# Kernel optimization log

Measured on AMD Instinct MI355X. Metric: run time of the kernel, lower is better.

The kernel has to match this reference:

```python
import jax, jax.numpy as jnp
import numpy as np
from jax import lax

B, T = 4, 2048
IN_CH, SKIP_CH, OUT_CH, K = 256, 128, 128, 5
N_MAMBA, D_STATE, D_CONV, EXPAND = 2, 16, 4, 2
D_INNER = EXPAND * OUT_CH
DT_RANK = (OUT_CH + 15) // 16  # ceil(d_model/16) = 8
L = 2 * T
EPS = 1e-5


def setup_inputs() -> dict:
    key = jax.random.key(0)
    ks = jax.random.split(key, 16)
    def rn(k, shape, s=0.02):
        return jax.random.normal(k, shape, jnp.float32) * s
    A_init = jnp.broadcast_to(jnp.arange(1, D_STATE + 1, dtype=jnp.float32),
                              (N_MAMBA, 2, D_INNER, D_STATE))
    return {
        'x': rn(ks[0], (B, IN_CH, T), 1.0),
        'skip': rn(ks[1], (B, SKIP_CH, L), 1.0),
        'up_w': rn(ks[2], (IN_CH, IN_CH, K)),       # torch ConvTranspose1d weight (in,out,k)
        'up_b': jnp.zeros((IN_CH,), jnp.float32),
        'fus_w': rn(ks[3], (OUT_CH, IN_CH + SKIP_CH)),  # 1x1 conv
        'fus_b': jnp.zeros((OUT_CH,), jnp.float32),
        'gn_w': jnp.ones((OUT_CH,), jnp.float32),
        'gn_b': jnp.zeros((OUT_CH,), jnp.float32),
        'prelu_a': jnp.array(0.25, jnp.float32),
        'ln_w': jnp.ones((N_MAMBA, OUT_CH), jnp.float32),
        'ln_b': jnp.zeros((N_MAMBA, OUT_CH), jnp.float32),
        'in_w': rn(ks[4], (N_MAMBA, 2, 2 * D_INNER, OUT_CH)),
        'conv_w': rn(ks[5], (N_MAMBA, 2, D_INNER, D_CONV), 0.1),
        'conv_b': jnp.zeros((N_MAMBA, 2, D_INNER), jnp.float32),
        'xproj_w': rn(ks[6], (N_MAMBA, 2, DT_RANK + 2 * D_STATE, D_INNER)),
        'dtproj_w': rn(ks[7], (N_MAMBA, 2, D_INNER, DT_RANK), 0.1),
        'dtproj_b': rn(ks[8], (N_MAMBA, 2, D_INNER), 0.1),
        'A_log': jnp.log(A_init),
        'Dp': jnp.ones((N_MAMBA, 2, D_INNER), jnp.float32),
        'out_w': rn(ks[9], (N_MAMBA, 2, OUT_CH, D_INNER)),
    }


def _mamba_branch(xn, cw, cb, iw, xw, dw, db, Alog, Dp, ow):
    # xn: [B, L, d_model] -> [B, L, d_model]; standard Mamba selective scan.
    xz = jnp.einsum('bld,ed->ble', xn, iw)            # [B,L,2*D_INNER]
    xi, z = jnp.split(xz, 2, axis=-1)
    # causal depthwise conv over time
    xc = lax.conv_general_dilated(xi.transpose(0, 2, 1), cw[:, None, :], (1,),
                                  [(D_CONV - 1, 0)], feature_group_count=D_INNER,
                                  dimension_numbers=('NCH', 'OIH', 'NCH'))
    xi = jax.nn.silu(xc + cb[None, :, None]).transpose(0, 2, 1)  # [B,L,D_INNER]
    dbl = jnp.einsum('bld,ed->ble', xi, xw)           # [B,L,DT_RANK+2N]
    dt = jax.nn.softplus(jnp.einsum('blr,dr->bld', dbl[..., :DT_RANK], dw) + db)
    Bc = dbl[..., DT_RANK:DT_RANK + D_STATE]          # [B,L,N]
    Cc = dbl[..., DT_RANK + D_STATE:]                 # [B,L,N]
    A = -jnp.exp(Alog)                                # [D_INNER,N]
    dA = jnp.exp(dt[..., None] * A)                   # [B,L,D_INNER,N]
    dBx = dt[..., None] * Bc[:, :, None, :] * xi[..., None]
    def comb(c1, c2):
        a1, b1 = c1
        a2, b2 = c2
        return a1 * a2, a2 * b1 + b2
    _, h = lax.associative_scan(comb, (dA, dBx), axis=1)  # h_t = dA_t h_{t-1} + dBx_t
    y = jnp.einsum('bldn,bln->bld', h, Cc) + Dp * xi
    return jnp.einsum('ble,de->bld', y * jax.nn.silu(z), ow)


def _forward(x, skip, up_w, up_b, fus_w, fus_b, gn_w, gn_b, prelu_a, ln_w, ln_b,
             in_w, conv_w, conv_b, xproj_w, dtproj_w, dtproj_b, A_log, Dp, out_w):
    p = K // 2
    # ConvTranspose1d(stride=2, padding=p, output_padding=1) == lhs-dilated conv with flipped kernel
    wt = jnp.flip(up_w, -1).transpose(1, 0, 2)        # (out,in,k)
    u = lax.conv_general_dilated(x, wt, (1,), [(K - 1 - p, K - 1 - p + 1)],
                                 lhs_dilation=(2,),
                                 dimension_numbers=('NCH', 'OIH', 'NCH'))
    u = u + up_b[None, :, None]
    u = u[..., :skip.shape[-1]]
    h = jnp.concatenate([u, skip], axis=1)            # [B, in+skip, L]
    h = jnp.einsum('bct,oc->bot', h, fus_w) + fus_b[None, :, None]
    # GroupNorm(1, C): normalize over (C,T) per sample
    mu = h.mean(axis=(1, 2), keepdims=True)
    var = h.var(axis=(1, 2), keepdims=True)
    h = (h - mu) / jnp.sqrt(var + EPS) * gn_w[None, :, None] + gn_b[None, :, None]
    h = jnp.where(h >= 0, h, prelu_a * h)             # PReLU (single param)
    h = h.transpose(0, 2, 1)                          # [B, L, C]
    for i in range(N_MAMBA):
        # BiMambaBlock: pre-LN, forward + time-reversed Mamba, residual sum
        mu2 = h.mean(-1, keepdims=True)
        v2 = h.var(-1, keepdims=True)
        xn = (h - mu2) / jnp.sqrt(v2 + EPS) * ln_w[i] + ln_b[i]
        f = _mamba_branch(xn, conv_w[i, 0], conv_b[i, 0], in_w[i, 0], xproj_w[i, 0],
                          dtproj_w[i, 0], dtproj_b[i, 0], A_log[i, 0], Dp[i, 0], out_w[i, 0])
        b = _mamba_branch(jnp.flip(xn, 1), conv_w[i, 1], conv_b[i, 1], in_w[i, 1], xproj_w[i, 1],
                          dtproj_w[i, 1], dtproj_b[i, 1], A_log[i, 1], Dp[i, 1], out_w[i, 1])
        h = h + f + jnp.flip(b, 1)
    return h.transpose(0, 2, 1)                       # [B, C_out, L]


def reference(x, skip, up_w, up_b, fus_w, fus_b, gn_w, gn_b, prelu_a, ln_w, ln_b,
              in_w, conv_w, conv_b, xproj_w, dtproj_w, dtproj_b, A_log, Dp, out_w):
    return _forward(x, skip, up_w, up_b, fus_w, fus_b, gn_w, gn_b, prelu_a, ln_w, ln_b,
                    in_w, conv_w, conv_b, xproj_w, dtproj_w, dtproj_b, A_log, Dp, out_w)
```

## Files before the change

kernel.cpp:

```cpp
#include <hip/hip_runtime.h>
#include <hip/hip_bf16.h>

#define Bsz 4
#define Tt 2048
#define Ll 4096
#define NC 256
#define CH 16
#define NG 16

typedef short bf16x8 __attribute__((ext_vector_type(8)));
typedef float f32x4 __attribute__((ext_vector_type(4)));
typedef float f32x2 __attribute__((ext_vector_type(2)));

static __device__ __forceinline__ f32x2 pk_fma(f32x2 a, f32x2 b, f32x2 c){
  f32x2 d;
  asm("v_pk_fma_f32 %0, %1, %2, %3" : "=v"(d) : "v"(a), "v"(b), "v"(c));
  return d;
}
static __device__ __forceinline__ f32x2 pk_mul(f32x2 a, f32x2 b){
  f32x2 d;
  asm("v_pk_mul_f32 %0, %1, %2" : "=v"(d) : "v"(a), "v"(b));
  return d;
}
static __device__ __forceinline__ f32x2 lo2(f32x4 v){ return (f32x2){v.x, v.y}; }
static __device__ __forceinline__ f32x2 hi2(f32x4 v){ return (f32x2){v.z, v.w}; }

static __device__ __forceinline__ float bs2f(unsigned short u){
  union{float f; unsigned int i;} v; v.i = ((unsigned int)u)<<16; return v.f;
}
static __device__ __forceinline__ unsigned short f2bs(float f){
  union{float f; unsigned int i;} v; v.f = f;
  unsigned int r = (v.i + 0x7fffu + ((v.i>>16)&1u)) >> 16;
  return (unsigned short)r;
}

__global__ void k_cvt(const float* __restrict__ src, unsigned short* __restrict__ dst, int n){
  int i = blockIdx.x*256 + threadIdx.x;
  if (i < n) dst[i] = f2bs(src[i]);
}

__global__ void k_prepx(const float* __restrict__ xw, unsigned short* __restrict__ wxb){
  int row = blockIdx.x, br = blockIdx.y, col = threadIdx.x;
  float v = (row < 40) ? xw[((size_t)br*40 + row)*256 + col] : 0.f;
  wxb[((size_t)br*64 + row)*256 + col] = f2bs(v);
}

__global__ void k_prepA(const float* __restrict__ Alog, float* __restrict__ AEX,
                        float* __restrict__ A0C, float* __restrict__ CHN){
  int br = blockIdx.x, d = threadIdx.x;
  float A[16];
  #pragma unroll
  for (int j=0;j<4;j++){
    float4 a4 = *(const float4*)&Alog[(size_t)br*4096 + d*16 + j*4];
    A[4*j]  = -__expf(a4.x); A[4*j+1] = -__expf(a4.y);
    A[4*j+2]= -__expf(a4.z); A[4*j+3] = -__expf(a4.w);
    *(float4*)&AEX[(size_t)br*4096 + d*16 + j*4] = (float4){A[4*j],A[4*j+1],A[4*j+2],A[4*j+3]};
  }
  bool chain = true;
  #pragma unroll
  for (int n=1;n<16;n++){
    float expect = A[0]*(float)(n+1);
    if (fabsf(A[n]-expect) > 1e-3f*fabsf(expect)) chain = false;
  }
  A0C[br*256 + d] = A[0];
  CHN[br*256 + d] = chain ? 1.f : 0.f;
}

__global__ void k_compose(const float* __restrict__ up_w, const float* __restrict__ fus_w,
                          const float* __restrict__ fus_b, const float* __restrict__ up_b,
                          unsigned short* __restrict__ WEb, unsigned short* __restrict__ WOb,
                          unsigned short* __restrict__ FWSb, float* __restrict__ BIAS2){
  int i = blockIdx.x;
  int o = threadIdx.x;
  float a0=0.f,a1=0.f,a2=0.f,a3=0.f,a4=0.f;
  for (int c=0;c<256;c++){
    float f = fus_w[o*384+c];
    const float* w = up_w + ((size_t)i*256+c)*5;
    a0 += f*w[0]; a1 += f*w[1]; a2 += f*w[2];
    a3 += f*w[3]; a4 += f*w[4];
  }
  WEb[(size_t)o*768 +       i] = f2bs(a4);
  WEb[(size_t)o*768 + 256 + i] = f2bs(a2);
  WEb[(size_t)o*768 + 512 + i] = f2bs(a0);
  WOb[(size_t)o*512 +       i] = f2bs(a3);
  WOb[(size_t)o*512 + 256 + i] = f2bs(a1);
  if (i<128) FWSb[o*128 + i] = f2bs(fus_w[o*384+256+i]);
  if (i==0){
    float bb = fus_b[o];
    for (int c=0;c<256;c++) bb += fus_w[o*384+c]*up_b[c];
    BIAS2[o]=bb;
  }
}

__global__ __launch_bounds__(256) void k_tx(const float* __restrict__ x, unsigned short* __restrict__ XT){
  __shared__ float tile[64][65];
  int b=blockIdx.z, t0=blockIdx.x*64, i0=blockIdx.y*64;
  int tid=threadIdx.x;
  for (int it=0;it<16;it++){
    int idx=it*256+tid; int ii=idx>>6, tt=idx&63;
    tile[ii][tt] = x[((size_t)b*256+i0+ii)*Tt + t0+tt];
  }
  __syncthreads();
  for (int it=0;it<16;it++){
    int idx=it*256+tid; int tt=idx>>6, ii=idx&63;
    XT[((size_t)b*2050 + t0+tt+1)*256 + i0+ii] = f2bs(tile[ii][tt]);
  }
}

__global__ void k_zero(unsigned short* __restrict__ XT){
  int tid=threadIdx.x;
  for (int b=0;b<Bsz;b++){
    XT[((size_t)b*2050)*256 + tid] = 0;
    XT[((size_t)b*2050+2049)*256 + tid] = 0;
  }
}

__global__ __launch_bounds__(256) void k_ts(const float* __restrict__ skip, unsigned short* __restrict__ SKT){
  __shared__ float tile[64][65];
  int b=blockIdx.z, l0=blockIdx.x*64, s0=blockIdx.y*64;
  int tid=threadIdx.x;
  for (int it=0;it<16;it++){
    int idx=it*256+tid; int ss=idx>>6, ll=idx&63;
    tile[ss][ll] = skip[((size_t)b*128+s0+ss)*Ll + l0+ll];
  }
  __syncthreads();
  for (int it=0;it<16;it++){
    int idx=it*256+tid; int ll=idx>>6, ss=idx&63;
    SKT[((size_t)b*Ll + l0+ll)*128 + s0+ss] = f2bs(tile[ss][ll]);
  }
}

__global__ __launch_bounds__(256) void k_up(const unsigned short* __restrict__ XT,
                     const unsigned short* __restrict__ SKT,
                     const unsigned short* __restrict__ WEb, const unsigned short* __restrict__ WOb,
                     const unsigned short* __restrict__ FWSb, const float* __restrict__ B2,
                     float* __restrict__ h0, float* __restrict__ gst){
  __shared__ unsigned short XL[66*264];
  __shared__ unsigned short Wb[128*72];
  __shared__ float red0[256], red1[256];
  int bt = blockIdx.x, par = blockIdx.y, b = blockIdx.z;
  int t0 = bt*64;
  int tid = threadIdx.x;
  int wave = tid>>6, lane = tid&63;
  int wm = wave>>1, wn = wave&1;
  int quad = lane>>4, l16 = lane&15;

  for (int idx=tid; idx<66*32; idx+=256){
    int row = idx>>5, c8 = idx&31;
    *(uint4*)&XL[row*264 + c8*8] = *(const uint4*)&XT[((size_t)b*2050 + t0 + row)*256 + c8*8];
  }

  const unsigned short* Wsrc = par ? WOb : WEb;
  const int Kw = par ? 512 : 768;
  const int tapbase = par ? 1 : 0;
  f32x4 acc[2][4];
  #pragma unroll
  for (int i=0;i<2;i++)
    #pragma unroll
    for (int j=0;j<4;j++) acc[i][j] = (f32x4){0.f,0.f,0.f,0.f};

  int nch = Kw>>6;
  for (int kc=0; kc<nch; kc++){
    __syncthreads();
    #pragma unroll
    for (int it=0; it<4; it++){
      int idx = it*256+tid;
      int row = idx>>3, c8 = idx&7;
      *(uint4*)&Wb[row*72 + c8*8] = *(const uint4*)&Wsrc[(size_t)row*Kw + kc*64 + c8*8];
    }
    __syncthreads();
    #pragma unroll
    for (int ks=0; ks<64; ks+=32){
      int kg = kc*64 + ks;
      int tap = kg>>8, ib = kg&255;
      bf16x8 af[2], bf[4];
      #pragma unroll
      for (int mt=0;mt<2;mt++)
        af[mt] = *(bf16x8*)&XL[(wm*32+mt*16+l16 + tapbase + tap)*264 + ib + quad*8];
      #pragma unroll
      for (int nt=0;nt<4;nt++)
        bf[nt] = *(bf16x8*)&Wb[(wn*64+nt*16+l16)*72 + ks + quad*8];
      #pragma unroll
      for (int mt=0;mt<2;mt++)
        #pragma unroll
        for (int nt=0;nt<4;nt++)
          acc[mt][nt] = __builtin_amdgcn_mfma_f32_16x16x32_bf16(af[mt], bf[nt], acc[mt][nt], 0,0,0);
    }
  }

  __syncthreads();
  for (int idx=tid; idx<64*16; idx+=256){
    int row = idx>>4, c8 = idx&15;
    *(uint4*)&XL[row*136 + c8*8] = *(const uint4*)&SKT[((size_t)b*Ll + 2*(t0+row)+par)*128 + c8*8];
  }
  for (int kc=0; kc<2; kc++){
    __syncthreads();
    #pragma unroll
    for (int it=0; it<4; it++){
      int idx = it*256+tid;
      int row = idx>>3, c8 = idx&7;
      *(uint4*)&Wb[row*72 + c8*8] = *(const uint4*)&FWSb[(size_t)row*128 + kc*64 + c8*8];
    }
    __syncthreads();
    #pragma unroll
    for (int ks=0; ks<64; ks+=32){
      bf16x8 af[2], bf[4];
      #pragma unroll
      for (int mt=0;mt<2;mt++)
        af[mt] = *(bf16x8*)&XL[(wm*32+mt*16+l16)*136 + kc*64 + ks + quad*8];
      #pragma unroll
      for (int nt=0;nt<4;nt++)
        bf[nt] = *(bf16x8*)&Wb[(wn*64+nt*16+l16)*72 + ks + quad*8];
      #pragma unroll
      for (int mt=0;mt<2;mt++)
        #pragma unroll
        for (int nt=0;nt<4;nt++)
          acc[mt][nt] = __builtin_amdgcn_mfma_f32_16x16x32_bf16(af[mt], bf[nt], acc[mt][nt], 0,0,0);
    }
  }

  float s1=0.f, s2=0.f;
  #pragma unroll
  for (int mt=0;mt<2;mt++)
    #pragma unroll
    for (int nt=0;nt<4;nt++)
      #pragma unroll
      for (int r=0;r<4;r++){
        int m = wm*32 + mt*16 + quad*4 + r;
        int lrow = 2*(t0+m) + par;
        int col = wn*64 + nt*16 + l16;
        float v = acc[mt][nt][r] + B2[col];
        h0[((size_t)b*Ll + lrow)*128 + col] = v;
        s1 += v; s2 += v*v;
      }
  red0[tid]=s1; red1[tid]=s2;
  __syncthreads();
  for (int st=128; st>0; st>>=1){
    if (tid<st){ red0[tid]+=red0[tid+st]; red1[tid]+=red1[tid+st]; }
    __syncthreads();
  }
  if (tid==0){ atomicAdd(&gst[b*2], red0[0]); atomicAdd(&gst[b*2+1], red1[0]); }
}

__global__ void k_gnfin(float* gst){
  int b = threadIdx.x;
  if (b < Bsz){
    float n = (float)Ll*128.f;
    float mu = gst[b*2]/n;
    float var = gst[b*2+1]/n - mu*mu;
    gst[8+b]=mu; gst[12+b]=rsqrtf(var+1e-5f);
  }
}

__global__ __launch_bounds__(256) void k_gnln(const float* __restrict__ h0, const float* __restrict__ gn_w,
                      const float* __restrict__ gn_b, const float* __restrict__ pa,
                      const float* __restrict__ gst, const float* __restrict__ lnw,
                      const float* __restrict__ lnb, float* __restrict__ hres,
                      unsigned short* __restrict__ xn){
  int row = blockIdx.x*4 + (threadIdx.x>>6);
  int lane = threadIdx.x & 63;
  int b = row >> 12;
  float mu_g = gst[8+b], inv_g = gst[12+b];
  float a = pa[0];
  const float* hp = h0 + (size_t)row*128;
  float u0 = (hp[lane]   -mu_g)*inv_g*gn_w[lane]    + gn_b[lane];
  float u1 = (hp[lane+64]-mu_g)*inv_g*gn_w[lane+64] + gn_b[lane+64];
  float v0 = u0>=0.f ? u0 : a*u0;
  float v1 = u1>=0.f ? u1 : a*u1;
  float* rp = hres + (size_t)row*128;
  rp[lane] = v0; rp[lane+64] = v1;
  float s = v0+v1, q = v0*v0+v1*v1;
  #pragma unroll
  for (int off=32; off>0; off>>=1){
    s += __shfl_xor(s, off, 64);
    q += __shfl_xor(q, off, 64);
  }
  float mu = s*(1.f/128.f);
  float rs = rsqrtf(q*(1.f/128.f)-mu*mu + 1e-5f);
  unsigned short* xp = xn + (size_t)row*128;
  xp[lane]    = f2bs((v0-mu)*rs*lnw[lane]    + lnb[lane]);
  xp[lane+64] = f2bs((v1-mu)*rs*lnw[lane+64] + lnb[lane+64]);
}

__global__ __launch_bounds__(256) void k_gemm_in(const unsigned short* __restrict__ A,
                          const unsigned short* __restrict__ W,
                          unsigned short* __restrict__ C){
  __shared__ unsigned short As[128*72];
  __shared__ unsigned short Bs[128*72];
  int tid = threadIdx.x;
  int row0 = blockIdx.x*128;
  int n0   = blockIdx.y*128;
  int dir  = blockIdx.z;
  const unsigned short* Wp = W + (size_t)dir*512*128;
  unsigned short* Cp = C + (size_t)dir*Bsz*Ll*512;
  int wave = tid>>6, lane = tid&63;
  int wm = wave>>1, wn = wave&1;
  int quad = lane>>4, l16 = lane&15;
  f32x4 acc[4][4];
  #pragma unroll
  for (int i=0;i<4;i++)
    #pragma unroll
    for (int j=0;j<4;j++) acc[i][j] = (f32x4){0.f,0.f,0.f,0.f};

  for (int kb=0; kb<128; kb+=64){
    __syncthreads();
    #pragma unroll
    for (int it=0; it<4; it++){
      int idx = it*256 + tid;
      int row = idx>>3, c8 = idx&7;
      int r = row0 + row;
      int p = r & (Ll-1); int bb = r >> 12;
      int src = (bb<<12) + (dir ? (Ll-1-p) : p);
      *(uint4*)&As[row*72 + c8*8] = *(const uint4*)&A[(size_t)src*128 + kb + c8*8];
      *(uint4*)&Bs[row*72 + c8*8] = *(const uint4*)&Wp[(size_t)(n0+row)*128 + kb + c8*8];
    }
    __syncthreads();
    #pragma unroll
    for (int ks=0; ks<64; ks+=32){
      bf16x8 af[4], bf[4];
      #pragma unroll
      for (int mt=0;mt<4;mt++)
        af[mt] = *(bf16x8*)&As[(wm*64+mt*16+l16)*72 + ks + quad*8];
      #pragma unroll
      for (int nt=0;nt<4;nt++)
        bf[nt] = *(bf16x8*)&Bs[(wn*64+nt*16+l16)*72 + ks + quad*8];
      #pragma unroll
      for (int mt=0;mt<4;mt++)
        #pragma unroll
        for (int nt=0;nt<4;nt++)
          acc[mt][nt] = __builtin_amdgcn_mfma_f32_16x16x32_bf16(af[mt], bf[nt], acc[mt][nt], 0,0,0);
    }
  }
  #pragma unroll
  for (int mt=0;mt<4;mt++)
    #pragma unroll
    for (int nt=0;nt<4;nt++)
      #pragma unroll
      for (int r=0;r<4;r++){
        int row = row0 + wm*64 + mt*16 + quad*4 + r;
        int col = n0 + wn*64 + nt*16 + l16;
        Cp[(size_t)row*512 + col] = f2bs(acc[mt][nt][r]);
      }
}

template<int DO_LN>
__global__ __launch_bounds__(256) void k_gemm_out_t(const unsigned short* __restrict__ Y,
                           const unsigned short* __restrict__ W,
                           float* __restrict__ C, const float* __restrict__ lnw,
                           const float* __restrict__ lnb, unsigned short* __restrict__ xn){
  __shared__ unsigned short As[64*72];
  __shared__ unsigned short Bs[128*72];
  __shared__ float redS[2][4][2][4][2][2];
  int tid = threadIdx.x;
  int row0 = blockIdx.x*64;
  int wave = tid>>6, lane = tid&63;
  int wm = wave>>1, wn = wave&1;
  int quad = lane>>4, l16 = lane&15;
  const size_t planeY = (size_t)Bsz*Ll*256;
  f32x4 acc[2][4];
  #pragma unroll
  for (int i=0;i<2;i++)
    #pragma unroll
    for (int j=0;j<4;j++) acc[i][j] = (f32x4){0.f,0.f,0.f,0.f};

  for (int kc=0; kc<8; kc++){
    int dirp = kc>>2;
    int kb = (kc&3)*64;
    const unsigned short* Wp = W + (size_t)dirp*128*256;
    __syncthreads();
    #pragma unroll
    for (int it=0; it<2; it++){
      int idx = it*256 + tid;
      int row = idx>>3, c8 = idx&7;
      int r = row0 + row;
      int p = r & (Ll-1); int bb = r >> 12;
      int srow = dirp ? ((bb<<12) + (Ll-1-p)) : r;
      *(uint4*)&As[row*72 + c8*8] = *(const uint4*)&Y[dirp*planeY + (size_t)srow*256 + kb + c8*8];
    }
    #pragma unroll
    for (int it=0; it<4; it++){
      int idx = it*256 + tid;
      int row = idx>>3, c8 = idx&7;
      *(uint4*)&Bs[row*72 + c8*8] = *(const uint4*)&Wp[(size_t)row*256 + kb + c8*8];
    }
    __syncthreads();
    #pragma unroll
    for (int ks=0; ks<64; ks+=32){
      bf16x8 af[2], bf[4];
      #pragma unroll
      for (int mt=0;mt<2;mt++)
        af[mt] = *(bf16x8*)&As[(wm*32+mt*16+l16)*72 + ks + quad*8];
      #pragma unroll
      for (int nt=0;nt<4;nt++)
        bf[nt] = *(bf16x8*)&Bs[(wn*64+nt*16+l16)*72 + ks + quad*8];
      #pragma unroll
      for (int mt=0;mt<2;mt++)
        #pragma unroll
        for (int nt=0;nt<4;nt++)
          acc[mt][nt] = __builtin_amdgcn_mfma_f32_16x16x32_bf16(af[mt], bf[nt], acc[mt][nt], 0,0,0);
    }
  }

  float vals[2][4][4];
  #pragma unroll
  for (int mt=0;mt<2;mt++)
    #pragma unroll
    for (int nt=0;nt<4;nt++)
      #pragma unroll
      for (int r=0;r<4;r++){
        int row = row0 + wm*32 + mt*16 + quad*4 + r;
        int col = wn*64 + nt*16 + l16;
        float v = C[(size_t)row*128 + col] + acc[mt][nt][r];
        C[(size_t)row*128 + col] = v;
        vals[mt][nt][r] = v;
      }

  if (DO_LN){
    #pragma unroll
    for (int mt=0;mt<2;mt++)
      #pragma unroll
      for (int r=0;r<4;r++){
        float s = 0.f, q = 0.f;
        #pragma unroll
        for (int nt=0;nt<4;nt++){ float v = vals[mt][nt][r]; s += v; q += v*v; }
        #pragma unroll
        for (int off=1; off<16; off<<=1){
          s += __shfl_xor(s, off, 64);
          q += __shfl_xor(q, off, 64);
        }
        if (l16 == 0){
          redS[wm][quad][mt][r][wn][0] = s;
          redS[wm][quad][mt][r][wn][1] = q;
        }
      }
    __syncthreads();
    #pragma unroll
    for (int mt=0;mt<2;mt++)
      #pragma unroll
      for (int r=0;r<4;r++){
        float s = redS[wm][quad][mt][r][0][0] + redS[wm][quad][mt][r][1][0];
        float q = redS[wm][quad][mt][r][0][1] + redS[wm][quad][mt][r][1][1];
        float mu = s*(1.f/128.f);
        float rs = rsqrtf(q*(1.f/128.f) - mu*mu + 1e-5f);
        int row = row0 + wm*32 + mt*16 + quad*4 + r;
        #pragma unroll
        for (int nt=0;nt<4;nt++){
          int col = wn*64 + nt*16 + l16;
          xn[(size_t)row*128 + col] = f2bs((vals[mt][nt][r]-mu)*rs*lnw[col] + lnb[col]);
        }
      }
  }
}

__global__ __launch_bounds__(256) void k_xproj3(const unsigned short* __restrict__ xz,
                        const unsigned short* __restrict__ wxb,
                        const float* __restrict__ cw, const float* __restrict__ cb,
                        unsigned short* __restrict__ xib, float* __restrict__ dbl){
  __shared__ unsigned short xiS[64*264];
  __shared__ unsigned short Bs[64*72];
  int tid = threadIdx.x;
  int dir = blockIdx.y;
  xz  += (size_t)dir*Bsz*Ll*512;
  wxb += (size_t)dir*64*256;
  cw  += dir*1024;
  cb  += dir*256;
  xib += (size_t)dir*Bsz*Ll*256;
  dbl += (size_t)dir*Bsz*Ll*40;
  size_t row0 = (size_t)blockIdx.x*64;
  int p0 = (int)(row0 & (Ll-1));

  {
    int d = tid;
    float4 w4 = *(const float4*)&cw[d*4];
    float bias = cb[d];
    float w0, w1, w2;
    if (p0 == 0){ w0=0.f; w1=0.f; w2=0.f; }
    else {
      w0 = bs2f(xz[(row0-3)*512 + d]);
      w1 = bs2f(xz[(row0-2)*512 + d]);
      w2 = bs2f(xz[(row0-1)*512 + d]);
    }
    #pragma unroll 4
    for (int rr=0; rr<64; rr++){
      float xv = bs2f(xz[(row0+rr)*512 + d]);
      float acc = bias + w4.x*w0 + w4.y*w1 + w4.z*w2 + w4.w*xv;
      float v = acc*__builtin_amdgcn_rcpf(1.f+__expf(-acc));
      unsigned short us = f2bs(v);
      xiS[rr*264 + d] = us;
      xib[(row0+rr)*256 + d] = us;
      w0=w1; w1=w2; w2=xv;
    }
  }

  int wave = tid>>6, lane = tid&63;
  int quad = lane>>4, l16 = lane&15;
  f32x4 acc[4];
  #pragma unroll
  for (int j=0;j<4;j++) acc[j] = (f32x4){0.f,0.f,0.f,0.f};

  for (int kb=0; kb<256; kb+=64){
    __syncthreads();
    #pragma unroll
    for (int it=0; it<2; it++){
      int idx = it*256 + tid;
      int row = idx>>3, c8 = idx&7;
      *(uint4*)&Bs[row*72 + c8*8] = *(const uint4*)&wxb[(size_t)row*256 + kb + c8*8];
    }
    __syncthreads();
    #pragma unroll
    for (int ks=0; ks<64; ks+=32){
      bf16x8 af = *(bf16x8*)&xiS[(wave*16+l16)*264 + kb + ks + quad*8];
      #pragma unroll
      for (int nt=0;nt<4;nt++){
        bf16x8 bf = *(bf16x8*)&Bs[(nt*16+l16)*72 + ks + quad*8];
        acc[nt] = __builtin_amdgcn_mfma_f32_16x16x32_bf16(af, bf, acc[nt], 0,0,0);
      }
    }
  }
  #pragma unroll
  for (int nt=0;nt<4;nt++)
    #pragma unroll
    for (int r=0;r<4;r++){
      int m = wave*16 + quad*4 + r;
      int col = nt*16 + l16;
      if (col < 40) dbl[(row0+m)*40 + col] = acc[nt][r];
    }
}

#define POWTREE2(e1, pw2) { \
  float _e2 = (e1)*(e1); \
  f32x2 _e2v = (f32x2){_e2,_e2}; \
  pw2[0] = (f32x2){(e1),_e2}; \
  pw2[1] = pk_mul(pw2[0], _e2v); \
  pw2[2] = pk_mul(pw2[1], _e2v); \
  pw2[3] = pk_mul(pw2[2], _e2v); \
  f32x2 _e8v = (f32x2){pw2[3].y, pw2[3].y}; \
  pw2[4] = pk_mul(pw2[0], _e8v); \
  pw2[5] = pk_mul(pw2[1], _e8v); \
  pw2[6] = pk_mul(pw2[2], _e8v); \
  pw2[7] = pk_mul(pw2[3], _e8v); }

__global__ __launch_bounds__(256) void k_scan1(const float* __restrict__ dbl,
                       const unsigned short* __restrict__ xib, const float* __restrict__ AEX,
                       const float* __restrict__ A0C, const float* __restrict__ CHNf,
                       const float* __restrict__ dtw, const float* __restrict__ dtb,
                       float* __restrict__ SD, float* __restrict__ Q){
  __shared__ float dblS[CH*24];
  int b = blockIdx.y, c = blockIdx.x, dir = blockIdx.z;
  int d = threadIdx.x;
  const float* dblP = dbl + (size_t)dir*Bsz*Ll*40;
  const unsigned short* xiP = xib + (size_t)dir*Bsz*Ll*256;
  size_t base = (size_t)b*Ll + (size_t)c*CH;
  if (d < CH*6){
    int p = d/6, j = d - p*6;
    *(float4*)&dblS[p*24 + j*4] = *(const float4*)&dblP[(base+p)*40 + j*4];
  }
  float A0 = A0C[dir*256 + d];
  bool chain = CHNf[dir*256 + d] != 0.f;
  f32x2 wv2[4];
  {
    const float* dw = dtw + (size_t)dir*2048 + d*8;
    float4 w0 = *(const float4*)&dw[0];
    float4 w1 = *(const float4*)&dw[4];
    wv2[0]=(f32x2){w0.x,w0.y}; wv2[1]=(f32x2){w0.z,w0.w};
    wv2[2]=(f32x2){w1.x,w1.y}; wv2[3]=(f32x2){w1.z,w1.w};
  }
  float bbt = dtb[dir*256 + d];
  __syncthreads();
  float sdt = 0.f;
  const unsigned short* xip = xiP + base*256 + d;
  size_t sbase = (size_t)dir*Bsz*NC*4096 + ((size_t)(b*NC + c))*4096 + (size_t)d*16;
  if (chain){
    bool n1 = fabsf(A0 + 1.f) < 1e-6f;
    float xv[CH];
    #pragma unroll
    for (int p=0;p<CH;p++) xv[p] = bs2f(xip[(size_t)p*256]);
    f32x2 h2[8];
    #pragma unroll
    for (int i=0;i<8;i++) h2[i] = (f32x2){0.f,0.f};
    #pragma unroll
    for (int p=0;p<CH;p++){
      const float* rw = &dblS[p*24];
      f32x4 t0 = *(const f32x4*)&rw[0];
      f32x4 t1 = *(const f32x4*)&rw[4];
      f32x2 dp = pk_mul(lo2(t0), wv2[0]);
      dp = pk_fma(hi2(t0), wv2[1], dp);
      dp = pk_fma(lo2(t1), wv2[2], dp);
      dp = pk_fma(hi2(t1), wv2[3], dp);
      float a0 = bbt + dp.x + dp.y;
      float t = __expf(a0);
      float u = 1.f + t;
      float dtv = (a0>20.f)? a0 : __logf(u);
      float e1 = n1 ? __builtin_amdgcn_rcpf(u) : __expf(dtv*A0);
      float dx = dtv*xv[p];
      sdt += dtv;
      f32x2 pw2[8];
      POWTREE2(e1, pw2);
      f32x2 dxv = (f32x2){dx,dx};
      f32x4 b0 = *(const f32x4*)&dblS[p*24+8];
      f32x4 b1 = *(const f32x4*)&dblS[p*24+12];
      f32x4 b2 = *(const f32x4*)&dblS[p*24+16];
      f32x4 b3 = *(const f32x4*)&dblS[p*24+20];
      h2[0] = pk_fma(pw2[0], h2[0], pk_mul(lo2(b0), dxv));
      h2[1] = pk_fma(pw2[1], h2[1], pk_mul(hi2(b0), dxv));
      h2[2] = pk_fma(pw2[2], h2[2], pk_mul(lo2(b1), dxv));
      h2[3] = pk_fma(pw2[3], h2[3], pk_mul(hi2(b1), dxv));
      h2[4] = pk_fma(pw2[4], h2[4], pk_mul(lo2(b2), dxv));
      h2[5] = pk_fma(pw2[5], h2[5], pk_mul(hi2(b2), dxv));
      h2[6] = pk_fma(pw2[6], h2[6], pk_mul(lo2(b3), dxv));
      h2[7] = pk_fma(pw2[7], h2[7], pk_mul(hi2(b3), dxv));
    }
    #pragma unroll
    for (int j=0;j<4;j++)
      *(float4*)&Q[sbase + 4*j] = (float4){h2[2*j].x,h2[2*j].y,h2[2*j+1].x,h2[2*j+1].y};
  } else {
    float A[16];
    #pragma unroll
    for (int j=0;j<4;j++)
      *(float4*)&A[4*j] = *(const float4*)&AEX[(size_t)dir*4096 + d*16 + j*4];
    float h[16];
    #pragma unroll
    for (int n=0;n<16;n++) h[n]=0.f;
    for (int p=0;p<CH;p++){
      const float* rw = &dblS[p*24];
      float4 t0 = *(const float4*)&rw[0], t1 = *(const float4*)&rw[4];
      float a0 = bbt + t0.x*wv2[0].x+t0.y*wv2[0].y+t0.z*wv2[1].x+t0.w*wv2[1].y
                     + t1.x*wv2[2].x+t1.y*wv2[2].y+t1.z*wv2[3].x+t1.w*wv2[3].y;
      float dtv = (a0>20.f)? a0 : __logf(1.f+__expf(a0));
      float xiv = bs2f(xip[(size_t)p*256]);
      float dx = dtv*xiv;
      sdt += dtv;
      float bc[16];
      *(float4*)&bc[0]  = *(const float4*)&rw[8];
      *(float4*)&bc[4]  = *(const float4*)&rw[12];
      *(float4*)&bc[8]  = *(const float4*)&rw[16];
      *(float4*)&bc[12] = *(const float4*)&rw[20];
      #pragma unroll
      for (int n=0;n<16;n++){
        float a = __expf(dtv*A[n]);
        h[n] = a*h[n] + bc[n]*dx;
      }
    }
    #pragma unroll
    for (int j=0;j<4;j++)
      *(float4*)&Q[sbase + 4*j] = (float4){h[4*j],h[4*j+1],h[4*j+2],h[4*j+3]};
  }
  SD[(((size_t)dir*Bsz + b)*NC + c)*256 + d] = sdt;
}

__global__ __launch_bounds__(64) void k_scan2a(float* __restrict__ SD, float* __restrict__ Q,
                        float* __restrict__ SDG, float* __restrict__ QG,
                        const float* __restrict__ AEX){
  int zb = blockIdx.z;
  int dir = zb >> 2;
  int g  = blockIdx.y;
  int t  = blockIdx.x*64 + threadIdx.x;
  int dn4 = t*4;
  int d = dn4 >> 4;
  float4 A4 = *(const float4*)&AEX[(size_t)dir*4096 + dn4];
  float* sd = SD + (((size_t)zb*NC) + (size_t)g*(NC/NG))*256 + d;
  float* q  = Q + (size_t)zb*NC*4096 + (size_t)g*(NC/NG)*4096 + dn4;
  float4 H = {0.f,0.f,0.f,0.f};
  float S = 0.f;
  #pragma unroll
  for (int c2=0; c2<NC/NG; c2++){
    float s_c = sd[(size_t)c2*256];
    float4 q_c = *(const float4*)(q + (size_t)c2*4096);
    sd[(size_t)c2*256] = S;
    *(float4*)(q + (size_t)c2*4096) = H;
    float4 p;
    p.x = __expf(A4.x*s_c); p.y = __expf(A4.y*s_c);
    p.z = __expf(A4.z*s_c); p.w = __expf(A4.w*s_c);
    H.x = p.x*H.x + q_c.x; H.y = p.y*H.y + q_c.y;
    H.z = p.z*H.z + q_c.z; H.w = p.w*H.w + q_c.w;
    S += s_c;
  }
  SDG[((size_t)zb*NG + g)*256 + d] = S;
  *(float4*)&QG[((size_t)zb*NG + g)*4096 + dn4] = H;
}

__global__ __launch_bounds__(64) void k_scan2b(const float* __restrict__ SDG, float* __restrict__ QG,
                        const float* __restrict__ AEX){
  int b = blockIdx.y, dir = blockIdx.z;
  int zb = dir*Bsz + b;
  int t = blockIdx.x*64 + threadIdx.x;
  int dn4 = t*4;
  int d = dn4 >> 4;
  float4 A4 = *(const float4*)&AEX[(size_t)dir*4096 + dn4];
  const float* sg = SDG + (size_t)zb*NG*256 + d;
  float* qg = QG + (size_t)zb*NG*4096 + dn4;
  float4 H = {0.f,0.f,0.f,0.f};
  #pragma unroll
  for (int g=0; g<NG; g++){
    float s = sg[(size_t)g*256];
    float4 qe = *(const float4*)(qg + (size_t)g*4096);
    *(float4*)(qg + (size_t)g*4096) = H;
    float4 p;
    p.x = __expf(A4.x*s); p.y = __expf(A4.y*s);
    p.z = __expf(A4.z*s); p.w = __expf(A4.w*s);
    H.x = p.x*H.x + qe.x; H.y = p.y*H.y + qe.y;
    H.z = p.z*H.z + qe.z; H.w = p.w*H.w + qe.w;
  }
}

__global__ __launch_bounds__(256) void k_scan3(const float* __restrict__ dbl,
                       unsigned short* xiy, const float* __restrict__ AEX,
                       const float* __restrict__ A0C, const float* __restrict__ CHNf,
                       const float* __restrict__ dtw, const float* __restrict__ dtb,
                       const float* __restrict__ Dpw, const float* __restrict__ Hs,
                       const float* __restrict__ SDp, const float* __restrict__ QG,
                       const unsigned short* __restrict__ xz){
  __shared__ float dblS[CH*40];
  int b = blockIdx.y, c = blockIdx.x, dir = blockIdx.z;
  int d = threadIdx.x;
  const float* dblP = dbl + (size_t)dir*Bsz*Ll*40;
  unsigned short* xiP = xiy + (size_t)dir*Bsz*Ll*256;
  const unsigned short* xzP = xz + (size_t)dir*Bsz*Ll*512;
  size_t base = (size_t)b*Ll + (size_t)c*CH;
  for (int idx=d; idx<CH*10; idx+=256){
    int p = idx/10, j = idx - p*10;
    *(float4*)&dblS[p*40 + j*4] = *(const float4*)&dblP[(base+p)*40 + j*4];
  }
  float A0 = A0C[dir*256 + d];
  bool chain = CHNf[dir*256 + d] != 0.f;
  f32x2 wv2[4];
  {
    const float* dw = dtw + (size_t)dir*2048 + d*8;
    float4 w0 = *(const float4*)&dw[0];
    float4 w1 = *(const float4*)&dw[4];
    wv2[0]=(f32x2){w0.x,w0.y}; wv2[1]=(f32x2){w0.z,w0.w};
    wv2[2]=(f32x2){w1.x,w1.y}; wv2[3]=(f32x2){w1.z,w1.w};
  }
  float bbt = dtb[dir*256 + d];
  float Dp = Dpw[dir*256 + d];
  int zb = dir*Bsz + b;
  size_t sbase = (size_t)zb*NC*4096 + (size_t)c*4096 + (size_t)d*16;
  float sdtp = SDp[(((size_t)zb)*NC + c)*256 + d];
  size_t gbase = ((size_t)zb*NG + (c >> 4))*4096 + (size_t)d*16;
  __syncthreads();
  unsigned short* xip = xiP + base*256 + d;
  const unsigned short* zp = xzP + base*512 + 256 + d;
  if (chain){
    bool n1 = fabsf(A0 + 1.f) < 1e-6f;
    float xv[CH], zv[CH];
    #pragma unroll
    for (int p=0;p<CH;p++) xv[p] = bs2f(xip[(size_t)p*256]);
    #pragma unroll
    for (int p=0;p<CH;p++) zv[p] = bs2f(zp[(size_t)p*512]);
    f32x2 h2[8];
    {
      float eg = __expf(A0*sdtp);
      f32x2 pg[8];
      POWTREE2(eg, pg);
      #pragma unroll
      for (int j=0;j<4;j++){
        float4 h4 = *(const float4*)&Hs[sbase + 4*j];
        float4 g4 = *(const float4*)&QG[gbase + 4*j];
        h2[2*j]   = pk_fma(pg[2*j],   (f32x2){g4.x,g4.y}, (f32x2){h4.x,h4.y});
        h2[2*j+1] = pk_fma(pg[2*j+1], (f32x2){g4.z,g4.w}, (f32x2){h4.z,h4.w});
      }
    }
    #pragma unroll
    for (int p=0;p<CH;p++){
      const float* rw = &dblS[p*40];
      f32x4 t0 = *(const f32x4*)&rw[0];
      f32x4 t1 = *(const f32x4*)&rw[4];
      f32x2 dp = pk_mul(lo2(t0), wv2[0]);
      dp = pk_fma(hi2(t0), wv2[1], dp);
      dp = pk_fma(lo2(t1), wv2[2], dp);
      dp = pk_fma(hi2(t1), wv2[3], dp);
      float a0 = bbt + dp.x + dp.y;
      float t = __expf(a0);
      float u = 1.f + t;
      float dtv = (a0>20.f)? a0 : __logf(u);
      float e1 = n1 ? __builtin_amdgcn_rcpf(u) : __expf(dtv*A0);
      float dx = dtv*xv[p];
      f32x2 pw2[8];
      POWTREE2(e1, pw2);
      f32x2 dxv = (f32x2){dx,dx};
      f32x4 b0 = *(const f32x4*)&dblS[p*40+8];
      f32x4 b1 = *(const f32x4*)&dblS[p*40+12];
      f32x4 b2 = *(const f32x4*)&dblS[p*40+16];
      f32x4 b3 = *(const f32x4*)&dblS[p*40+20];
      f32x4 c0 = *(const f32x4*)&dblS[p*40+24];
      f32x4 c1 = *(const f32x4*)&dblS[p*40+28];
      f32x4 c2 = *(const f32x4*)&dblS[p*40+32];
      f32x4 c3 = *(const f32x4*)&dblS[p*40+36];
      f32x2 ya;
      h2[0] = pk_fma(pw2[0], h2[0], pk_mul(lo2(b0), dxv));
      ya = pk_mul(h2[0], lo2(c0));
      h2[1] = pk_fma(pw2[1], h2[1], pk_mul(hi2(b0), dxv));
      ya = pk_fma(h2[1], hi2(c0), ya);
      h2[2] = pk_fma(pw2[2], h2[2], pk_mul(lo2(b1), dxv));
      ya = pk_fma(h2[2], lo2(c1), ya);
      h2[3] = pk_fma(pw2[3], h2[3], pk_mul(hi2(b1), dxv));
      ya = pk_fma(h2[3], hi2(c1), ya);
      h2[4] = pk_fma(pw2[4], h2[4], pk_mul(lo2(b2), dxv));
      ya = pk_fma(h2[4], lo2(c2), ya);
      h2[5] = pk_fma(pw2[5], h2[5], pk_mul(hi2(b2), dxv));
      ya = pk_fma(h2[5], hi2(c2), ya);
      h2[6] = pk_fma(pw2[6], h2[6], pk_mul(lo2(b3), dxv));
      ya = pk_fma(h2[6], lo2(c3), ya);
      h2[7] = pk_fma(pw2[7], h2[7], pk_mul(hi2(b3), dxv));
      ya = pk_fma(h2[7], hi2(c3), ya);
      float acc = ya.x + ya.y;
      float z = zv[p];
      float g = z*__builtin_amdgcn_rcpf(1.f+__expf(-z));
      xip[(size_t)p*256] = f2bs((acc + Dp*xv[p])*g);
    }
  } else {
    float A[16];
    #pragma unroll
    for (int j=0;j<4;j++)
      *(float4*)&A[4*j] = *(const float4*)&AEX[(size_t)dir*4096 + d*16 + j*4];
    float h[16];
    #pragma unroll
    for (int j=0;j<4;j++){
      float4 h4 = *(const float4*)&Hs[sbase + 4*j];
      float4 g4 = *(const float4*)&QG[gbase + 4*j];
      h[4*j]   = __expf(A[4*j]*sdtp)*g4.x   + h4.x;
      h[4*j+1] = __expf(A[4*j+1]*sdtp)*g4.y + h4.y;
      h[4*j+2] = __expf(A[4*j+2]*sdtp)*g4.z + h4.z;
      h[4*j+3] = __expf(A[4*j+3]*sdtp)*g4.w + h4.w;
    }
    for (int p=0;p<CH;p++){
      const float* rw = &dblS[p*40];
      float4 t0 = *(const float4*)&rw[0], t1 = *(const float4*)&rw[4];
      float a0 = bbt + t0.x*wv2[0].x+t0.y*wv2[0].y+t0.z*wv2[1].x+t0.w*wv2[1].y
                     + t1.x*wv2[2].x+t1.y*wv2[2].y+t1.z*wv2[3].x+t1.w*wv2[3].y;
      float dtv = (a0>20.f)? a0 : __logf(1.f+__expf(a0));
      float xiv = bs2f(xip[(size_t)p*256]);
      float dx = dtv*xiv;
      float bc[16], cc[16];
      *(float4*)&bc[0]  = *(const float4*)&rw[8];
      *(float4*)&bc[4]  = *(const float4*)&rw[12];
      *(float4*)&bc[8]  = *(const float4*)&rw[16];
      *(float4*)&bc[12] = *(const float4*)&rw[20];
      *(float4*)&cc[0]  = *(const float4*)&rw[24];
      *(float4*)&cc[4]  = *(const float4*)&rw[28];
      *(float4*)&cc[8]  = *(const float4*)&rw[32];
      *(float4*)&cc[12] = *(const float4*)&rw[36];
      float acc = 0.f;
      #pragma unroll
      for (int n=0;n<16;n++){
        float a = __expf(dtv*A[n]);
        h[n] = a*h[n] + bc[n]*dx;
        acc += h[n]*cc[n];
      }
      float z = bs2f(zp[(size_t)p*512]);
      float g = z*__builtin_amdgcn_rcpf(1.f+__expf(-z));
      xip[(size_t)p*256] = f2bs((acc + Dp*xiv)*g);
    }
  }
}

__global__ __launch_bounds__(256) void k_final(const float* __restrict__ hres, float* __restrict__ out){
  __shared__ float tile[64*129];
  int b = blockIdx.y, l0 = blockIdx.x*64;
  int tid = threadIdx.x;
  for (int q=0;q<32;q++){
    int idx = q*256 + tid;
    int l = idx >> 7, c = idx & 127;
    tile[l*129 + c] = hres[((size_t)b*Ll + l0 + l)*128 + c];
  }
  __syncthreads();
  int lo = tid & 63; int cbase = tid >> 6;
  for (int q=0;q<32;q++){
    int c = cbase + q*4;
    out[((size_t)b*128 + c)*Ll + l0 + lo] = tile[lo*129 + c];
  }
}

extern "C" void kernel_launch(void* const* d_in, const int* in_sizes, int n_in,
                              void* d_out, int out_size, void* d_ws, size_t ws_size,
                              hipStream_t stream){
  const float* x      = (const float*)d_in[0];
  const float* skip   = (const float*)d_in[1];
  const float* up_w   = (const float*)d_in[2];
  const float* up_b   = (const float*)d_in[3];
  const float* fus_w  = (const float*)d_in[4];
  const float* fus_b  = (const float*)d_in[5];
  const float* gn_w   = (const float*)d_in[6];
  const float* gn_b   = (const float*)d_in[7];
  const float* pa     = (const float*)d_in[8];
  const float* ln_w   = (const float*)d_in[9];
  const float* ln_b   = (const float*)d_in[10];
  const float* in_w   = (const float*)d_in[11];
  const float* conv_w = (const float*)d_in[12];
  const float* conv_b = (const float*)d_in[13];
  const float* xproj_w= (const float*)d_in[14];
  const float* dtproj_w=(const float*)d_in[15];
  const float* dtproj_b=(const float*)d_in[16];
  const float* A_log  = (const float*)d_in[17];
  const float* Dp     = (const float*)d_in[18];
  const float* out_w  = (const float*)d_in[19];

  float* w = (float*)d_ws;
  size_t off=0;
  float* B2 = w+off; off += 128;
  float* GST= w+off; off += 16;
  off = (off+3)&~(size_t)3;
  float* HR = w+off; off += (size_t)Bsz*Ll*128;
  float* DBL2= w+off; off += 2*(size_t)Bsz*Ll*40;
  unsigned short* XNB = (unsigned short*)(w+off); off += (size_t)Bsz*Ll*128/2;
  unsigned short* XZB2= (unsigned short*)(w+off); off += 2*(size_t)Bsz*Ll*512/2;
  unsigned short* IWB = (unsigned short*)(w+off); off += 2*2*512*128/2;
  unsigned short* OWB = (unsigned short*)(w+off); off += 2*2*128*256/2;
  unsigned short* WXB = (unsigned short*)(w+off); off += 2*2*64*256/2;
  unsigned short* WEb = (unsigned short*)(w+off); off += 768*128/2;
  unsigned short* WOb = (unsigned short*)(w+off); off += 512*128/2;
  unsigned short* FWSb= (unsigned short*)(w+off); off += 128*128/2;
  float* AEXb = w+off; off += 4*4096;
  float* A0Cb = w+off; off += 4*256;
  float* CHNb = w+off; off += 4*256;
  float* SDGb = w+off; off += (size_t)2*Bsz*NG*256;
  size_t planeS = (size_t)Bsz*NC*4096;
  float* U1 = w+off; off += 2*planeS;
  unsigned short* XT  = (unsigned short*)U1;
  unsigned short* SKT = (unsigned short*)(U1 + 1049604);
  float* SQ = U1;
  float* SD = (float*)XNB;
  float* QG = SD + 524288;
  float* U2 = w+off; off += 2*(size_t)Bsz*Ll*128;
  float* H0 = U2;
  unsigned short* XIB2 = (unsigned short*)U2;

  hipMemsetAsync(GST, 0, 16*sizeof(float), stream);
  k_cvt<<<(2*2*512*128+255)/256,256,0,stream>>>(in_w, IWB, 2*2*512*128);
  k_cvt<<<(2*2*128*256+255)/256,256,0,stream>>>(out_w, OWB, 2*2*128*256);
  k_prepx<<<dim3(64,4),256,0,stream>>>(xproj_w, WXB);
  k_prepA<<<4,256,0,stream>>>(A_log, AEXb, A0Cb, CHNb);
  k_compose<<<256,128,0,stream>>>(up_w, fus_w, fus_b, up_b, WEb, WOb, FWSb, B2);
  k_tx<<<dim3(Tt/64, 4, Bsz),256,0,stream>>>(x, XT);
  k_zero<<<1,256,0,stream>>>(XT);
  k_ts<<<dim3(Ll/64, 2, Bsz),256,0,stream>>>(skip, SKT);
  k_up<<<dim3(32, 2, Bsz),256,0,stream>>>(XT, SKT, WEb, WOb, FWSb, B2, H0, GST);
  k_gnfin<<<1,64,0,stream>>>(GST);
  k_gnln<<<Bsz*Ll/4,256,0,stream>>>(H0, gn_w, gn_b, pa, GST, ln_w, ln_b, HR, XNB);
  for (int i=0;i<2;i++){
    k_gemm_in<<<dim3(128,4,2),256,0,stream>>>(XNB, IWB + (size_t)(i*2)*512*128, XZB2);
    k_xproj3<<<dim3(Bsz*Ll/64,2),256,0,stream>>>(XZB2, WXB + (size_t)(i*2)*64*256,
                                                 conv_w + (i*2)*1024, conv_b + (i*2)*256,
                                                 XIB2, DBL2);
    k_scan1<<<dim3(NC,Bsz,2),256,0,stream>>>(DBL2, XIB2, AEXb + (size_t)(i*2)*4096,
                                             A0Cb + (i*2)*256, CHNb + (i*2)*256,
                                             dtproj_w + (i*2)*2048, dtproj_b + (i*2)*256, SD, SQ);
    k_scan2a<<<dim3(16,NG,2*Bsz),64,0,stream>>>(SD, SQ, SDGb, QG, AEXb + (size_t)(i*2)*4096);
    k_scan2b<<<dim3(16,Bsz,2),64,0,stream>>>(SDGb, QG, AEXb + (size_t)(i*2)*4096);
    k_scan3<<<dim3(NC,Bsz,2),256,0,stream>>>(DBL2, XIB2, AEXb + (size_t)(i*2)*4096,
                                             A0Cb + (i*2)*256, CHNb + (i*2)*256,
                                             dtproj_w + (i*2)*2048, dtproj_b + (i*2)*256,
                                             Dp + (i*2)*256, SQ, SD, QG, XZB2);
    if (i==0)
      k_gemm_out_t<1><<<256,256,0,stream>>>(XIB2, OWB + 0, HR, ln_w + 128, ln_b + 128, XNB);
    else
      k_gemm_out_t<0><<<256,256,0,stream>>>(XIB2, OWB + (size_t)2*128*256, HR,
                                            (const float*)nullptr, (const float*)nullptr,
                                            (unsigned short*)nullptr);
  }
  k_final<<<dim3(Ll/64,Bsz),256,0,stream>>>(HR, (float*)d_out);
}
```

Before: 393.9 us.

## Move SiLU gating into out-projection GEMM and fold small prep kernels

The z-gate (y*silu(z)) moves out of the scan3 kernel and into the A-tile load of the output GEMM, so scan3 no longer reads z and does less per-step work. The two weight conversions are merged into one launch, the zeroing of the XT pad rows moves into the transpose kernel, and the group-norm finalize is recomputed inside the gnln kernel. Together these cut kernel launches and scan-side memory traffic, in exchange for extra z reads and transcendental work in the GEMM load path. The intermediate y is now rounded to bf16 before gating, which slightly changes numerics.

After: 410.9 us. 4.3% more time.

```diff
diff --git a/kernel.cpp b/kernel.cpp
--- a/kernel.cpp
+++ b/kernel.cpp
@@ -34,9 +34,25 @@
   return (unsigned short)r;
 }
 
-__global__ void k_cvt(const float* __restrict__ src, unsigned short* __restrict__ dst, int n){
+static __device__ __forceinline__ unsigned int gate2(unsigned int yy, unsigned int zz){
+  float y0 = bs2f((unsigned short)(yy & 0xffffu));
+  float y1 = bs2f((unsigned short)(yy >> 16));
+  float z0 = bs2f((unsigned short)(zz & 0xffffu));
+  float z1 = bs2f((unsigned short)(zz >> 16));
+  float g0 = z0*__builtin_amdgcn_rcpf(1.f+__expf(-z0));
+  float g1 = z1*__builtin_amdgcn_rcpf(1.f+__expf(-z1));
+  return (unsigned int)f2bs(y0*g0) | ((unsigned int)f2bs(y1*g1) << 16);
+}
+
+__global__ void k_cvt2(const float* __restrict__ a, const float* __restrict__ b,
+                       unsigned short* __restrict__ da, unsigned short* __restrict__ db,
+                       int na, int nb){
   int i = blockIdx.x*256 + threadIdx.x;
-  if (i < n) dst[i] = f2bs(src[i]);
+  if (i < na) da[i] = f2bs(a[i]);
+  else {
+    int j = i - na;
+    if (j < nb) db[j] = f2bs(b[j]);
+  }
 }
 
 __global__ void k_prepx(const float* __restrict__ xw, unsigned short* __restrict__ wxb){
@@ -96,6 +112,10 @@
   __shared__ float tile[64][65];
   int b=blockIdx.z, t0=blockIdx.x*64, i0=blockIdx.y*64;
   int tid=threadIdx.x;
+  if (blockIdx.x==0 && blockIdx.y==0){
+    XT[((size_t)b*2050)*256 + tid] = 0;
+    XT[((size_t)b*2050+2049)*256 + tid] = 0;
+  }
   for (int it=0;it<16;it++){
     int idx=it*256+tid; int ii=idx>>6, tt=idx&63;
     tile[ii][tt] = x[((size_t)b*256+i0+ii)*Tt + t0+tt];
@@ -104,14 +124,6 @@
   for (int it=0;it<16;it++){
     int idx=it*256+tid; int tt=idx>>6, ii=idx&63;
     XT[((size_t)b*2050 + t0+tt+1)*256 + i0+ii] = f2bs(tile[ii][tt]);
-  }
-}
-
-__global__ void k_zero(unsigned short* __restrict__ XT){
-  int tid=threadIdx.x;
-  for (int b=0;b<Bsz;b++){
-    XT[((size_t)b*2050)*256 + tid] = 0;
-    XT[((size_t)b*2050+2049)*256 + tid] = 0;
   }
 }
 
@@ -242,16 +254,6 @@
   if (tid==0){ atomicAdd(&gst[b*2], red0[0]); atomicAdd(&gst[b*2+1], red1[0]); }
 }
 
-__global__ void k_gnfin(float* gst){
-  int b = threadIdx.x;
-  if (b < Bsz){
-    float n = (float)Ll*128.f;
-    float mu = gst[b*2]/n;
-    float var = gst[b*2+1]/n - mu*mu;
-    gst[8+b]=mu; gst[12+b]=rsqrtf(var+1e-5f);
-  }
-}
-
 __global__ __launch_bounds__(256) void k_gnln(const float* __restrict__ h0, const float* __restrict__ gn_w,
                       const float* __restrict__ gn_b, const float* __restrict__ pa,
                       const float* __restrict__ gst, const float* __restrict__ lnw,
@@ -260,7 +262,10 @@
   int row = blockIdx.x*4 + (threadIdx.x>>6);
   int lane = threadIdx.x & 63;
   int b = row >> 12;
-  float mu_g = gst[8+b], inv_g = gst[12+b];
+  const float ninv = 1.f/((float)Ll*128.f);
+  float mu_g = gst[b*2]*ninv;
+  float var_g = gst[b*2+1]*ninv - mu_g*mu_g;
+  float inv_g = rsqrtf(var_g + 1e-5f);
   float a = pa[0];
   const float* hp = h0 + (size_t)row*128;
   float u0 = (hp[lane]   -mu_g)*inv_g*gn_w[lane]    + gn_b[lane];
@@ -345,6 +350,7 @@
 
 template<int DO_LN>
 __global__ __launch_bounds__(256) void k_gemm_out_t(const unsigned short* __restrict__ Y,
+                           const unsigned short* __restrict__ XZ,
                            const unsigned short* __restrict__ W,
                            float* __restrict__ C, const float* __restrict__ lnw,
                            const float* __restrict__ lnb, unsigned short* __restrict__ xn){
@@ -357,6 +363,7 @@
   int wm = wave>>1, wn = wave&1;
   int quad = lane>>4, l16 = lane&15;
   const size_t planeY = (size_t)Bsz*Ll*256;
+  const size_t planeXZ = (size_t)Bsz*Ll*512;
   f32x4 acc[2][4];
   #pragma unroll
   for (int i=0;i<2;i++)
@@ -375,7 +382,12 @@
       int r = row0 + row;
       int p = r & (Ll-1); int bb = r >> 12;
       int srow = dirp ? ((bb<<12) + (Ll-1-p)) : r;
-      *(uint4*)&As[row*72 + c8*8] = *(const uint4*)&Y[dirp*planeY + (size_t)srow*256 + kb + c8*8];
+      uint4 y8 = *(const uint4*)&Y[dirp*planeY + (size_t)srow*256 + kb + c8*8];
+      uint4 z8 = *(const uint4*)&XZ[dirp*planeXZ + (size_t)srow*512 + 256 + kb + c8*8];
+      uint4 o;
+      o.x = gate2(y8.x, z8.x); o.y = gate2(y8.y, z8.y);
+      o.z = gate2(y8.z, z8.z); o.w = gate2(y8.w, z8.w);
+      *(uint4*)&As[row*72 + c8*8] = o;
     }
     #pragma unroll
     for (int it=0; it<4; it++){
@@ -708,14 +720,12 @@
                        const float* __restrict__ A0C, const float* __restrict__ CHNf,
                        const float* __restrict__ dtw, const float* __restrict__ dtb,
                        const float* __restrict__ Dpw, const float* __restrict__ Hs,
-                       const float* __restrict__ SDp, const float* __restrict__ QG,
-                       const unsigned short* __restrict__ xz){
+                       const float* __restrict__ SDp, const float* __restrict__ QG){
   __shared__ float dblS[CH*40];
   int b = blockIdx.y, c = blockIdx.x, dir = blockIdx.z;
   int d = threadIdx.x;
   const float* dblP = dbl + (size_t)dir*Bsz*Ll*40;
   unsigned short* xiP = xiy + (size_t)dir*Bsz*Ll*256;
-  const unsigned short* xzP = xz + (size_t)dir*Bsz*Ll*512;
   size_t base = (size_t)b*Ll + (size_t)c*CH;
   for (int idx=d; idx<CH*10; idx+=256){
     int p = idx/10, j = idx - p*10;
@@ -739,14 +749,11 @@
   size_t gbase = ((size_t)zb*NG + (c >> 4))*4096 + (size_t)d*16;
   __syncthreads();
   unsigned short* xip = xiP + base*256 + d;
-  const unsigned short* zp = xzP + base*512 + 256 + d;
   if (chain){
     bool n1 = fabsf(A0 + 1.f) < 1e-6f;
-    float xv[CH], zv[CH];
+    float xv[CH];
     #pragma unroll
     for (int p=0;p<CH;p++) xv[p] = bs2f(xip[(size_t)p*256]);
-    #pragma unroll
-    for (int p=0;p<CH;p++) zv[p] = bs2f(zp[(size_t)p*512]);
     f32x2 h2[8];
     {
       float eg = __expf(A0*sdtp);
@@ -804,9 +811,7 @@
       h2[7] = pk_fma(pw2[7], h2[7], pk_mul(hi2(b3), dxv));
       ya = pk_fma(h2[7], hi2(c3), ya);
       float acc = ya.x + ya.y;
-      float z = zv[p];
-      float g = z*__builtin_amdgcn_rcpf(1.f+__expf(-z));
-      xip[(size_t)p*256] = f2bs((acc + Dp*xv[p])*g);
+      xip[(size_t)p*256] = f2bs(acc + Dp*xv[p]);
     }
   } else {
     float A[16];
@@ -847,9 +852,7 @@
         h[n] = a*h[n] + bc[n]*dx;
         acc += h[n]*cc[n];
       }
-      float z = bs2f(zp[(size_t)p*512]);
-      float g = z*__builtin_amdgcn_rcpf(1.f+__expf(-z));
-      xip[(size_t)p*256] = f2bs((acc + Dp*xiv)*g);
+      xip[(size_t)p*256] = f2bs(acc + Dp*xiv);
     }
   }
 }
@@ -926,16 +929,14 @@
   unsigned short* XIB2 = (unsigned short*)U2;
 
   hipMemsetAsync(GST, 0, 16*sizeof(float), stream);
-  k_cvt<<<(2*2*512*128+255)/256,256,0,stream>>>(in_w, IWB, 2*2*512*128);
-  k_cvt<<<(2*2*128*256+255)/256,256,0,stream>>>(out_w, OWB, 2*2*128*256);
+  k_cvt2<<<(2*2*512*128 + 2*2*128*256 + 255)/256,256,0,stream>>>(in_w, out_w, IWB, OWB,
+                                                                 2*2*512*128, 2*2*128*256);
   k_prepx<<<dim3(64,4),256,0,stream>>>(xproj_w, WXB);
   k_prepA<<<4,256,0,stream>>>(A_log, AEXb, A0Cb, CHNb);
   k_compose<<<256,128,0,stream>>>(up_w, fus_w, fus_b, up_b, WEb, WOb, FWSb, B2);
   k_tx<<<dim3(Tt/64, 4, Bsz),256,0,stream>>>(x, XT);
-  k_zero<<<1,256,0,stream>>>(XT);
   k_ts<<<dim3(Ll/64, 2, Bsz),256,0,stream>>>(skip, SKT);
   k_up<<<dim3(32, 2, Bsz),256,0,stream>>>(XT, SKT, WEb, WOb, FWSb, B2, H0, GST);
-  k_gnfin<<<1,64,0,stream>>>(GST);
   k_gnln<<<Bsz*Ll/4,256,0,stream>>>(H0, gn_w, gn_b, pa, GST, ln_w, ln_b, HR, XNB);
   for (int i=0;i<2;i++){
     k_gemm_in<<<dim3(128,4,2),256,0,stream>>>(XNB, IWB + (size_t)(i*2)*512*128, XZB2);
@@ -950,11 +951,11 @@
     k_scan3<<<dim3(NC,Bsz,2),256,0,stream>>>(DBL2, XIB2, AEXb + (size_t)(i*2)*4096,
                                              A0Cb + (i*2)*256, CHNb + (i*2)*256,
                                              dtproj_w + (i*2)*2048, dtproj_b + (i*2)*256,
-                                             Dp + (i*2)*256, SQ, SD, QG, XZB2);
+                                             Dp + (i*2)*256, SQ, SD, QG);
     if (i==0)
-      k_gemm_out_t<1><<<256,256,0,stream>>>(XIB2, OWB + 0, HR, ln_w + 128, ln_b + 128, XNB);
+      k_gemm_out_t<1><<<256,256,0,stream>>>(XIB2, XZB2, OWB + 0, HR, ln_w + 128, ln_b + 128, XNB);
     else
-      k_gemm_out_t<0><<<256,256,0,stream>>>(XIB2, OWB + (size_t)2*128*256, HR,
+      k_gemm_out_t<0><<<256,256,0,stream>>>(XIB2, XZB2, OWB + (size_t)2*128*256, HR,
                                             (const float*)nullptr, (const float*)nullptr,
                                             (unsigned short*)nullptr);
   }
```
